# Kernel tuning notes

Hardware: AMD Instinct MI355X
Metric: run time of the kernel (lower is better)

## Reference

```python
import jax, jax.numpy as jnp
import numpy as np

N = 200000      # nodes per graph
E = 6400000     # edges per graph
F_IN = 100      # node feature dim (GCNConv(100,16))
HID = 16
NC = 2
STRIDE = 20     # log_softmax(...)[::20]
M = N // STRIDE # rows fed to the MLP head


def _gcn(x, src, dst, W1, b1, W2, b2):
    """PyG-style GCNConv x2: add self loops, sym-normalize, linear -> aggregate -> bias."""
    n = x.shape[0]
    loops = jnp.arange(n)
    s = jnp.concatenate([src, loops])
    d = jnp.concatenate([dst, loops])
    deg = jax.ops.segment_sum(jnp.ones(s.shape[0], dtype=x.dtype), d, num_segments=n)
    dinv = jnp.where(deg > 0, jax.lax.rsqrt(deg), 0.0)
    norm = (dinv[s] * dinv[d])[:, None]  # [E+n, 1]
    h = x @ W1                                    # [n, 16]
    h = jax.ops.segment_sum(norm * h[s], d, num_segments=n) + b1
    h = jax.nn.relu(h)  # dropout is identity in eval mode
    h = h @ W2                                    # [n, 2]
    h = jax.ops.segment_sum(norm * h[s], d, num_segments=n) + b2
    return jax.nn.log_softmax(h, axis=1)[::STRIDE]  # [n/20, 2]


def setup_inputs() -> dict:
    key = jax.random.key(0)
    ks = jax.random.split(key, 24)
    inp = {
        'batch1_edge_index': jax.random.randint(ks[0], (2, E), 0, N),
        'batch1_x': jax.random.normal(ks[1], (N, F_IN), dtype=jnp.float32),
        'batch2_edge_index': jax.random.randint(ks[2], (2, E), 0, N),
        'batch2_x': jax.random.normal(ks[3], (N, F_IN), dtype=jnp.float32),
        'transE_input': jax.random.uniform(ks[4], (M,), dtype=jnp.float32),
        'ComplEx_input': jax.random.uniform(ks[5], (M,), dtype=jnp.float32),
        'path_input': jax.random.uniform(ks[6], (M,), dtype=jnp.float32),
        'edit_input': jax.random.uniform(ks[7], (M,), dtype=jnp.float32),
    }
    s = 0.1
    inp['gh_W1'] = jax.random.normal(ks[8], (F_IN, HID), dtype=jnp.float32) * s
    inp['gh_b1'] = jnp.zeros((HID,), dtype=jnp.float32)
    inp['gh_W2'] = jax.random.normal(ks[9], (HID, NC), dtype=jnp.float32) * s
    inp['gh_b2'] = jnp.zeros((NC,), dtype=jnp.float32)
    inp['gt_W1'] = jax.random.normal(ks[10], (F_IN, HID), dtype=jnp.float32) * s
    inp['gt_b1'] = jnp.zeros((HID,), dtype=jnp.float32)
    inp['gt_W2'] = jax.random.normal(ks[11], (HID, NC), dtype=jnp.float32) * s
    inp['gt_b2'] = jnp.zeros((NC,), dtype=jnp.float32)
    inp['m_W1'] = jax.random.normal(ks[12], (5, 80), dtype=jnp.float32) * s
    inp['m_b1'] = jnp.zeros((80,), dtype=jnp.float32)
    inp['m_W2'] = jax.random.normal(ks[13], (80, 10), dtype=jnp.float32) * s
    inp['m_b2'] = jnp.zeros((10,), dtype=jnp.float32)
    inp['m_W3'] = jax.random.normal(ks[14], (10, 1), dtype=jnp.float32) * s
    inp['m_b3'] = jnp.zeros((1,), dtype=jnp.float32)
    return inp


def reference(batch1_edge_index, batch1_x, batch2_edge_index, batch2_x,
              transE_input, ComplEx_input, path_input, edit_input,
              gh_W1, gh_b1, gh_W2, gh_b2,
              gt_W1, gt_b1, gt_W2, gt_b2,
              m_W1, m_b1, m_W2, m_b2, m_W3, m_b3):
    gcnh_out = _gcn(batch1_x, batch1_edge_index[0], batch1_edge_index[1],
                    gh_W1, gh_b1, gh_W2, gh_b2)
    # gcnt_out is computed in the original forward but never used in the output
    gcnt_out = _gcn(batch2_x, batch2_edge_index[0], batch2_edge_index[1],
                    gt_W1, gt_b1, gt_W2, gt_b2)
    BP_input = jnp.concatenate(
        [transE_input[:, None], ComplEx_input[:, None], path_input[:, None], gcnh_out], axis=1)  # [M, 5]
    # NOTE: original computes mean/std normalization then OVERWRITES it with
    # min_max_normalize(BP_input); we faithfully apply only global min-max.
    mn, mx = jnp.min(BP_input), jnp.max(BP_input)
    BP_norm = (BP_input - mn) / (mx - mn)
    h = jax.nn.relu(BP_norm @ m_W1 + m_b1)
    h = jax.nn.relu(h @ m_W2 + m_b2)
    out = jax.nn.sigmoid(h @ m_W3 + m_b3)  # [M, 1]
    return out
```

## Files before the change

### kernel.cpp

```cpp
#include <hip/hip_runtime.h>
#include <math.h>

#define NN 200000
#define NE 6400000
#define FIN 100
#define MR 10000
#define BSH 14
#define NBK 13
#define NSB 1563
#define EPB 4096
#define CAP1E 544768
#define SBB 133
#define CAP2E 4864
#define SCAP 360448
#define STCAP 5120

static __device__ __forceinline__ unsigned enc_f(float f){
  unsigned u = __float_as_uint(f);
  return (u & 0x80000000u) ? ~u : (u | 0x80000000u);
}
static __device__ __forceinline__ float dec_f(unsigned u){
  return (u & 0x80000000u) ? __uint_as_float(u ^ 0x80000000u) : __uint_as_float(~u);
}
static __device__ __forceinline__ unsigned short f2bf(float f){
  unsigned u = __float_as_uint(f);
  return (unsigned short)((u + 0x7fffu + ((u >> 16) & 1u)) >> 16);
}
static __device__ __forceinline__ float bf2f(unsigned short h){
  return __uint_as_float(((unsigned)h) << 16);
}
static __device__ __forceinline__ float bflo(unsigned u){ return bf2f((unsigned short)u); }
static __device__ __forceinline__ float bfhi(unsigned u){ return bf2f((unsigned short)(u>>16)); }

__global__ void k_init(int* bcur1, int* bcur2, float* gacc, unsigned* mm, unsigned* scnt){
  int i = blockIdx.x*blockDim.x + threadIdx.x;
  if(i < NBK) bcur1[i] = i*CAP1E;
  if(i < NSB) bcur2[i] = i*CAP2E;
  if(i < 2*MR) gacc[i] = 0.f;
  if(i == 0){ mm[0] = 0xFFFFFFFFu; mm[1] = 0u; scnt[0] = 0u; }
}

__global__ __launch_bounds__(256) void k_stageA(const int* __restrict__ src,
                                                const int* __restrict__ dst,
                                                int* __restrict__ bcur1,
                                                unsigned* __restrict__ bucket1){
  __shared__ unsigned stage[EPB];
  __shared__ unsigned char binOf[EPB];
  __shared__ int cnt[4][NBK];
  __shared__ int tot[NBK], bst[NBK], woff[4][NBK], gbase[NBK];
  int t = threadIdx.x;
  int w = t >> 6;
  int ebase = blockIdx.x*EPB;
  int nEdge = min(EPB, NE - ebase);
  if(t < 4*NBK) ((int*)cnt)[t] = 0;
  __syncthreads();
  unsigned pk[16]; int bb[16], rr[16];
  const int4* s4 = (const int4*)(src + ebase);
  const int4* d4 = (const int4*)(dst + ebase);
  #pragma unroll
  for(int j=0;j<4;j++){
    int q = t + j*256, eo = q*4;
    if(eo < nEdge){
      int4 s = s4[q]; int4 d = d4[q];
      int ds[4] = {d.x,d.y,d.z,d.w}, ss[4] = {s.x,s.y,s.z,s.w};
      #pragma unroll
      for(int k=0;k<4;k++){
        int b = ds[k]>>BSH;
        pk[j*4+k] = ((unsigned)(ds[k] & 16383) << 18) | (unsigned)ss[k];
        bb[j*4+k] = b;
        rr[j*4+k] = atomicAdd(&cnt[w][b], 1);
      }
    } else {
      rr[j*4+0]=rr[j*4+1]=rr[j*4+2]=rr[j*4+3] = -1;
    }
  }
  __syncthreads();
  if(t < NBK){
    int s = 0;
    #pragma unroll
    for(int wv=0; wv<4; wv++){ woff[wv][t] = s; s += cnt[wv][t]; }
    tot[t] = s;
  }
  __syncthreads();
  if(t == 0){
    int run = 0;
    #pragma unroll
    for(int b=0;b<NBK;b++){ bst[b] = run; run += tot[b]; }
  }
  __syncthreads();
  if(t < NBK && tot[t]) gbase[t] = atomicAdd(&bcur1[t], tot[t]);
  #pragma unroll
  for(int j=0;j<16;j++){
    if(rr[j] >= 0){
      int b = bb[j];
      int p = bst[b] + woff[w][b] + rr[j];
      stage[p] = pk[j]; binOf[p] = (unsigned char)b;
    }
  }
  __syncthreads();
  for(int k=t; k<nEdge; k+=256){
    int b = binOf[k];
    bucket1[gbase[b] + (k - bst[b])] = stage[k];
  }
}

__global__ __launch_bounds__(256) void k_stageB(const unsigned* __restrict__ bucket1,
                                                const int* __restrict__ bcur1,
                                                int* __restrict__ bcur2,
                                                unsigned* __restrict__ bucket2,
                                                unsigned* __restrict__ sed,
                                                unsigned* __restrict__ scnt){
  __shared__ unsigned stage[EPB];
  __shared__ unsigned char binOf[EPB];
  __shared__ int cnt[128], bst[128], gbase[128];
  __shared__ unsigned sbuf[384];
  __shared__ int slds, sgbase;
  int t = threadIdx.x;
  int b = blockIdx.x / SBB;
  int chunk = blockIdx.x % SBB;
  int cntb = bcur1[b] - b*CAP1E;
  int el = chunk*EPB;
  int nEdge = min(EPB, cntb - el);
  if(nEdge <= 0) return;
  if(t < 128) cnt[t] = 0;
  if(t == 0) slds = 0;
  __syncthreads();
  int t20 = (20 - (4*b) % 20) % 20;
  unsigned pk2[16]; int ln[16], rr[16];
  const uint4* e4 = (const uint4*)(bucket1 + (size_t)b*CAP1E + el);
  #pragma unroll
  for(int j=0;j<4;j++){
    int q = t + j*256, eo = q*4;
    uint4 e = make_uint4(0,0,0,0);
    if(eo < nEdge) e = e4[q];
    unsigned ev[4] = {e.x, e.y, e.z, e.w};
    #pragma unroll
    for(int k=0;k<4;k++){
      int idx = j*4+k;
      if(eo + k < nEdge){
        unsigned p = ev[k];
        unsigned dl14 = p >> 18;
        int bin = (int)(dl14 >> 7);
        pk2[idx] = ((dl14 & 127u) << 18) | (p & 0x3FFFFu);
        ln[idx] = bin;
        rr[idx] = atomicAdd(&cnt[bin], 1);
        if((int)(dl14 % 20u) == t20){
          int sp = atomicAdd(&slds, 1);
          if(sp < 384){
            unsigned sidx = (unsigned)((b*16384 + (int)dl14) / 20);
            sbuf[sp] = (sidx << 18) | (p & 0x3FFFFu);
          }
        }
      } else rr[idx] = -1;
    }
  }
  __syncthreads();
  if(t == 0){
    int run = 0;
    for(int i=0;i<128;i++){ bst[i] = run; run += cnt[i]; }
    if(slds > 384) slds = 384;
    sgbase = (slds > 0) ? (int)atomicAdd(scnt, (unsigned)slds) : 0;
  }
  __syncthreads();
  if(t < 128 && cnt[t]){
    int sbg = (b<<7) + t;
    gbase[t] = atomicAdd(&bcur2[sbg], cnt[t]);
  }
  #pragma unroll
  for(int j=0;j<16;j++){
    if(rr[j] >= 0){
      int p = bst[ln[j]] + rr[j];
      stage[p] = pk2[j]; binOf[p] = (unsigned char)ln[j];
    }
  }
  __syncthreads();
  for(int k=t; k<nEdge; k+=256){
    int bin = binOf[k];
    bucket2[gbase[bin] + (k - bst[bin])] = stage[k];
  }
  for(int k=t; k<slds; k+=256){
    int gp = sgbase + k;
    if(gp < SCAP) sed[gp] = sbuf[k];
  }
}

__global__ __launch_bounds__(256) void k_cnt(const unsigned* __restrict__ bucket2,
                                             const int* __restrict__ bcur2,
                                             float* __restrict__ dinv){
  __shared__ int c[128];
  int sb = blockIdx.x, t = threadIdx.x;
  if(t < 128) c[t] = 0;
  __syncthreads();
  int e0 = sb*CAP2E, e1 = bcur2[sb];
  for(int i=e0+t; i<e1; i+=256){
    unsigned pkv = bucket2[i];
    atomicAdd(&c[pkv>>18], 1);
  }
  __syncthreads();
  if(t < 128){
    int g = sb*128 + t;
    if(g < NN) dinv[g] = rsqrtf((float)(c[t] + 1));
  }
}

__global__ __launch_bounds__(256) void k_xw1(const float* __restrict__ x,
                                             const float* __restrict__ W1,
                                             const float* __restrict__ dinv,
                                             unsigned short* __restrict__ h1b){
  int row = blockIdx.x*256 + threadIdx.x;
  if(row >= NN) return;
  const float4* xr = (const float4*)(x + (size_t)row*FIN);
  float acc[16];
  #pragma unroll
  for(int c=0;c<16;c++) acc[c] = 0.f;
  #pragma unroll 5
  for(int kk=0;kk<25;kk++){
    float4 xv = xr[kk];
    const float* w = W1 + kk*4*16;
    #pragma unroll
    for(int c=0;c<16;c++){
      acc[c] += xv.x*w[c] + xv.y*w[16+c] + xv.z*w[32+c] + xv.w*w[48+c];
    }
  }
  float dv = dinv[row];
  unsigned p[8];
  #pragma unroll
  for(int c=0;c<8;c++){
    p[c] = (unsigned)f2bf(acc[2*c]*dv) | ((unsigned)f2bf(acc[2*c+1]*dv) << 16);
  }
  uint4* o = (uint4*)(h1b + (size_t)row*16);
  o[0] = make_uint4(p[0],p[1],p[2],p[3]);
  o[1] = make_uint4(p[4],p[5],p[6],p[7]);
}

__global__ __launch_bounds__(512) void k_aggfused(const unsigned* __restrict__ bucket2,
                                                  const int* __restrict__ bcur2,
                                                  const float* __restrict__ dinv,
                                                  const unsigned short* __restrict__ h1b,
                                                  const float* __restrict__ b1,
                                                  const float* __restrict__ W2,
                                                  float* __restrict__ h2s){
  __shared__ unsigned srt[STCAP];
  __shared__ int cnt[128], coff[129], cur[128];
  __shared__ int wsum0;
  int t = threadIdx.x, sb = blockIdx.x;
  int e0 = sb*CAP2E, e1 = bcur2[sb];
  int n  = e1 - e0;
  bool ok = (n <= STCAP);
  if(t < 128) cnt[t] = 0;
  __syncthreads();

  if(ok){
    unsigned er[10];
    #pragma unroll
    for(int k=0;k<10;k++){
      int i = e0 + t + k*512;
      if(i < e1){
        unsigned p = bucket2[i];
        er[k] = p;
        atomicAdd(&cnt[p>>18], 1);
      } else er[k] = 0xFFFFFFFFu;
    }
    __syncthreads();
    int v = (t<128) ? cnt[t] : 0;
    int s = v;
    #pragma unroll
    for(int o=1;o<64;o<<=1){
      int u = __shfl_up(s, o, 64);
      if((t&63) >= o) s += u;
    }
    if(t == 63) wsum0 = s;
    __syncthreads();
    if(t < 128){
      int ex = s - v + ((t>=64) ? wsum0 : 0);
      coff[t] = ex; cur[t] = ex;
    }
    if(t == 0) coff[128] = n;
    __syncthreads();
    #pragma unroll
    for(int k=0;k<10;k++){
      if(er[k] != 0xFFFFFFFFu){
        int p = atomicAdd(&cur[er[k]>>18], 1);
        srt[p] = er[k] & 0x3FFFFu;
      }
    }
    __syncthreads();

    int node = t>>2, q = (t>>1)&1, f = t&1;
    int g = sb*128 + node;
    bool live = (g < NN);
    int s0 = 0, s1 = 0;
    if(live){ s0 = coff[node]; s1 = coff[node+1]; }
    int ne = s1 - s0;
    int mid = s0 + ((ne+1)>>1);
    int jb = q ? mid : s0;
    int je = q ? s1 : mid;
    const uint4* h1q = (const uint4*)h1b;
    float acc[8];
    #pragma unroll
    for(int c=0;c<8;c++) acc[c] = 0.f;
    if(live && q==0){
      uint4 su = h1q[(size_t)g*2 + f];
      acc[0]=bflo(su.x); acc[1]=bfhi(su.x); acc[2]=bflo(su.y); acc[3]=bfhi(su.y);
      acc[4]=bflo(su.z); acc[5]=bfhi(su.z); acc[6]=bflo(su.w); acc[7]=bfhi(su.w);
    }
    if(live){
      int j = jb;
      for(; j+4 <= je; j+=4){
        unsigned a0=srt[j], a1=srt[j+1], a2=srt[j+2], a3=srt[j+3];
        uint4 u0=h1q[a0*2+f], u1=h1q[a1*2+f], u2=h1q[a2*2+f], u3=h1q[a3*2+f];
        acc[0] += (bflo(u0.x)+bflo(u1.x)) + (bflo(u2.x)+bflo(u3.x));
        acc[1] += (bfhi(u0.x)+bfhi(u1.x)) + (bfhi(u2.x)+bfhi(u3.x));
        acc[2] += (bflo(u0.y)+bflo(u1.y)) + (bflo(u2.y)+bflo(u3.y));
        acc[3] += (bfhi(u0.y)+bfhi(u1.y)) + (bfhi(u2.y)+bfhi(u3.y));
        acc[4] += (bflo(u0.z)+bflo(u1.z)) + (bflo(u2.z)+bflo(u3.z));
        acc[5] += (bfhi(u0.z)+bfhi(u1.z)) + (bfhi(u2.z)+bfhi(u3.z));
        acc[6] += (bflo(u0.w)+bflo(u1.w)) + (bflo(u2.w)+bflo(u3.w));
        acc[7] += (bfhi(u0.w)+bfhi(u1.w)) + (bfhi(u2.w)+bfhi(u3.w));
      }
      for(; j<je; j++){
        uint4 u = h1q[srt[j]*2+f];
        acc[0]+=bflo(u.x); acc[1]+=bfhi(u.x); acc[2]+=bflo(u.y); acc[3]+=bfhi(u.y);
        acc[4]+=bflo(u.z); acc[5]+=bfhi(u.z); acc[6]+=bflo(u.w); acc[7]+=bfhi(u.w);
      }
    }
    #pragma unroll
    for(int c=0;c<8;c++) acc[c] += __shfl_xor(acc[c], 2, 4);
    if(live){
      float dvd = dinv[g];
      float p0 = 0.f, p1 = 0.f;
      #pragma unroll
      for(int c=0;c<8;c++){
        int fc = f*8 + c;
        float r = fmaxf(dvd*acc[c] + b1[fc], 0.f);
        p0 += r*W2[fc*2+0];
        p1 += r*W2[fc*2+1];
      }
      p0 += __shfl_xor(p0, 1, 4);
      p1 += __shfl_xor(p1, 1, 4);
      if((t&3) == 0){
        h2s[g*2+0] = dvd * p0;
        h2s[g*2+1] = dvd * p1;
      }
    }
  } else {
    float* accf = (float*)srt;
    for(int i=t; i<2048; i+=512) accf[i] = 0.f;
    __syncthreads();
    int grp = t>>4, f = t&15;
    for(int i=e0+grp; i<e1; i+=32){
      unsigned pkv = bucket2[i];
      atomicAdd(&accf[(pkv>>18)*16 + f], bf2f(h1b[(size_t)(pkv & 0x3FFFFu)*16 + f]));
    }
    __syncthreads();
    for(int nd=grp; nd<128; nd+=32){
      int g = sb*128 + nd;
      if(g >= NN) continue;
      float dvd = dinv[g];
      float acc = accf[nd*16 + f] + bf2f(h1b[(size_t)g*16 + f]);
      float r = fmaxf(dvd*acc + b1[f], 0.f);
      float p0 = r * W2[f*2+0];
      float p1 = r * W2[f*2+1];
      #pragma unroll
      for(int o=8;o>0;o>>=1){
        p0 += __shfl_xor(p0, o, 16);
        p1 += __shfl_xor(p1, o, 16);
      }
      if(f == 0){
        h2s[g*2+0] = dvd * p0;
        h2s[g*2+1] = dvd * p1;
      }
    }
  }
}

__global__ __launch_bounds__(256) void k_agg2s(const unsigned* __restrict__ sed,
                                               const unsigned* __restrict__ scnt,
                                               const float* __restrict__ h2s,
                                               float* __restrict__ gacc){
  int total = (int)scnt[0];
  if(total > SCAP) total = SCAP;
  const float2* h2v = (const float2*)h2s;
  for(int i = blockIdx.x*256 + threadIdx.x; i < total; i += gridDim.x*256){
    unsigned p = sed[i];
    int idx = (int)(p >> 18);
    int srcn = (int)(p & 0x3FFFFu);
    float2 v = h2v[srcn];
    atomicAdd(&gacc[idx*2+0], v.x);
    atomicAdd(&gacc[idx*2+1], v.y);
  }
}

__global__ __launch_bounds__(256) void k_post(const float* __restrict__ gacc,
                                              const float* __restrict__ h2s,
                                              const float* __restrict__ dinv,
                                              const float* __restrict__ b2,
                                              const float* __restrict__ t1,
                                              const float* __restrict__ t2,
                                              const float* __restrict__ t3,
                                              float* __restrict__ gout,
                                              unsigned* __restrict__ mm){
  int i = blockIdx.x*256 + threadIdx.x;
  float lo = 3.4e38f, hi = -3.4e38f;
  if(i < MR){
    int g = i*20;
    float dvd = dinv[g];
    float o0 = dvd*(gacc[i*2+0] + h2s[g*2+0]) + b2[0];
    float o1 = dvd*(gacc[i*2+1] + h2s[g*2+1]) + b2[1];
    float m = fmaxf(o0, o1);
    float lse = m + logf(expf(o0-m) + expf(o1-m));
    float g0 = o0 - lse, g1 = o1 - lse;
    gout[i*2+0] = g0; gout[i*2+1] = g1;
    float a = t1[i], bb = t2[i], c = t3[i];
    lo = fminf(fminf(a,bb), fminf(c, fminf(g0,g1)));
    hi = fmaxf(fmaxf(a,bb), fmaxf(c, fmaxf(g0,g1)));
  }
  #pragma unroll
  for(int o=32;o>0;o>>=1){
    lo = fminf(lo, __shfl_xor(lo, o, 64));
    hi = fmaxf(hi, __shfl_xor(hi, o, 64));
  }
  __shared__ float slo[4], shi[4];
  int w = threadIdx.x >> 6, l = threadIdx.x & 63;
  if(l == 0){ slo[w] = lo; shi[w] = hi; }
  __syncthreads();
  if(threadIdx.x == 0){
    for(int j=1;j<4;j++){ lo = fminf(lo, slo[j]); hi = fmaxf(hi, shi[j]); }
    atomicMin(&mm[0], enc_f(lo));
    atomicMax(&mm[1], enc_f(hi));
  }
}

__global__ __launch_bounds__(256) void k_mlp(const float* __restrict__ t1, const float* __restrict__ t2,
                                             const float* __restrict__ t3, const float* __restrict__ g,
                                             const unsigned* __restrict__ mm,
                                             const float* __restrict__ W1, const float* __restrict__ b1,
                                             const float* __restrict__ W2, const float* __restrict__ b2,
                                             const float* __restrict__ W3, const float* __restrict__ b3,
                                             float* __restrict__ out){
  int i = blockIdx.x*256 + threadIdx.x;
  if(i >= MR) return;
  float mn = dec_f(mm[0]), mx = dec_f(mm[1]);
  float sc = 1.f/(mx - mn);
  float in[5];
  in[0] = (t1[i]   - mn)*sc;
  in[1] = (t2[i]   - mn)*sc;
  in[2] = (t3[i]   - mn)*sc;
  in[3] = (g[2*i]  - mn)*sc;
  in[4] = (g[2*i+1]- mn)*sc;
  float a[80];
  #pragma unroll
  for(int j=0;j<80;j++){
    float s = b1[j];
    #pragma unroll
    for(int k=0;k<5;k++) s += in[k]*W1[k*80+j];
    a[j] = fmaxf(s, 0.f);
  }
  float h[10];
  #pragma unroll
  for(int j=0;j<10;j++){
    float s = b2[j];
    #pragma unroll
    for(int k=0;k<80;k++) s += a[k]*W2[k*10+j];
    h[j] = fmaxf(s, 0.f);
  }
  float o = b3[0];
  #pragma unroll
  for(int k=0;k<10;k++) o += h[k]*W3[k];
  out[i] = 1.f/(1.f + expf(-o));
}

extern "C" void kernel_launch(void* const* d_in, const int* in_sizes, int n_in,
                              void* d_out, int out_size, void* d_ws, size_t ws_size,
                              hipStream_t stream) {
  (void)in_sizes; (void)n_in; (void)out_size; (void)ws_size;
  const int*   eidx    = (const int*)  d_in[0];
  const int*   src     = eidx;
  const int*   dst     = eidx + NE;
  const float* x       = (const float*)d_in[1];
  const float* transE  = (const float*)d_in[4];
  const float* ComplEx = (const float*)d_in[5];
  const float* path    = (const float*)d_in[6];
  const float* ghW1    = (const float*)d_in[8];
  const float* ghb1    = (const float*)d_in[9];
  const float* ghW2    = (const float*)d_in[10];
  const float* ghb2    = (const float*)d_in[11];
  const float* mW1     = (const float*)d_in[16];
  const float* mb1     = (const float*)d_in[17];
  const float* mW2     = (const float*)d_in[18];
  const float* mb2     = (const float*)d_in[19];
  const float* mW3     = (const float*)d_in[20];
  const float* mb3     = (const float*)d_in[21];
  float* out = (float*)d_out;

  char* w = (char*)d_ws;
  size_t off = 0;
  auto alloc = [&](size_t bytes)->void*{
    void* p = w + off;
    off += (bytes + 255) & ~(size_t)255;
    return p;
  };
  unsigned* bucket1 = (unsigned*)alloc((size_t)NBK*CAP1E*4);
  unsigned* bucket2 = (unsigned*)alloc((size_t)NSB*CAP2E*4);
  float*    dinv    = (float*)   alloc((size_t)NN*4);
  unsigned short* h1b = (unsigned short*)alloc((size_t)NN*16*2);
  float*    h2s     = (float*)   alloc((size_t)NN*2*4);
  float*    gacc    = (float*)   alloc((size_t)MR*2*4);
  float*    gout    = (float*)   alloc((size_t)MR*2*4);
  unsigned* sed     = (unsigned*)alloc((size_t)SCAP*4);
  int*      bcur1   = (int*)     alloc(64*4);
  int*      bcur2   = (int*)     alloc((size_t)(NSB+1)*4);
  unsigned* mm      = (unsigned*)alloc(256);
  unsigned* scnt    = (unsigned*)alloc(256);

  const int SA_BLOCKS = (NE + EPB - 1)/EPB;
  const int SB_BLOCKS = NBK*SBB;

  k_init    <<<(2*MR+255)/256, 256, 0, stream>>>(bcur1, bcur2, gacc, mm, scnt);
  k_stageA  <<<SA_BLOCKS, 256, 0, stream>>>(src, dst, bcur1, bucket1);
  k_stageB  <<<SB_BLOCKS, 256, 0, stream>>>(bucket1, bcur1, bcur2, bucket2, sed, scnt);
  k_cnt     <<<NSB, 256, 0, stream>>>(bucket2, bcur2, dinv);
  k_xw1     <<<(NN+255)/256, 256, 0, stream>>>(x, ghW1, dinv, h1b);
  k_aggfused<<<NSB, 512, 0, stream>>>(bucket2, bcur2, dinv, h1b, ghb1, ghW2, h2s);
  k_agg2s   <<<512, 256, 0, stream>>>(sed, scnt, h2s, gacc);
  k_post    <<<(MR+255)/256, 256, 0, stream>>>(gacc, h2s, dinv, ghb2,
                                               transE, ComplEx, path, gout, mm);
  k_mlp     <<<(MR+255)/256, 256, 0, stream>>>(transE, ComplEx, path, gout, mm,
                                               mW1, mb1, mW2, mb2, mW3, mb3, out);
}
```

Baseline: 447.1 us.

## Compute degrees with global atomics in stageA and drop the separate count kernel

Measured after the change: 658.8 us. 47.4% more time.

```diff
diff --git a/kernel.cpp b/kernel.cpp
--- a/kernel.cpp
+++ b/kernel.cpp
@@ -32,18 +32,21 @@
 static __device__ __forceinline__ float bflo(unsigned u){ return bf2f((unsigned short)u); }
 static __device__ __forceinline__ float bfhi(unsigned u){ return bf2f((unsigned short)(u>>16)); }
 
-__global__ void k_init(int* bcur1, int* bcur2, float* gacc, unsigned* mm, unsigned* scnt){
+__global__ void k_init(int* bcur1, int* bcur2, float* gacc, unsigned* mm, unsigned* scnt,
+                       int* deg){
   int i = blockIdx.x*blockDim.x + threadIdx.x;
   if(i < NBK) bcur1[i] = i*CAP1E;
   if(i < NSB) bcur2[i] = i*CAP2E;
   if(i < 2*MR) gacc[i] = 0.f;
+  if(i < NN) deg[i] = 0;
   if(i == 0){ mm[0] = 0xFFFFFFFFu; mm[1] = 0u; scnt[0] = 0u; }
 }
 
 __global__ __launch_bounds__(256) void k_stageA(const int* __restrict__ src,
                                                 const int* __restrict__ dst,
                                                 int* __restrict__ bcur1,
-                                                unsigned* __restrict__ bucket1){
+                                                unsigned* __restrict__ bucket1,
+                                                int* __restrict__ deg){
   __shared__ unsigned stage[EPB];
   __shared__ unsigned char binOf[EPB];
   __shared__ int cnt[4][NBK];
@@ -69,6 +72,7 @@
         pk[j*4+k] = ((unsigned)(ds[k] & 16383) << 18) | (unsigned)ss[k];
         bb[j*4+k] = b;
         rr[j*4+k] = atomicAdd(&cnt[w][b], 1);
+        atomicAdd(&deg[ds[k]], 1);
       }
     } else {
       rr[j*4+0]=rr[j*4+1]=rr[j*4+2]=rr[j*4+3] = -1;
@@ -184,28 +188,9 @@
   }
 }
 
-__global__ __launch_bounds__(256) void k_cnt(const unsigned* __restrict__ bucket2,
-                                             const int* __restrict__ bcur2,
-                                             float* __restrict__ dinv){
-  __shared__ int c[128];
-  int sb = blockIdx.x, t = threadIdx.x;
-  if(t < 128) c[t] = 0;
-  __syncthreads();
-  int e0 = sb*CAP2E, e1 = bcur2[sb];
-  for(int i=e0+t; i<e1; i+=256){
-    unsigned pkv = bucket2[i];
-    atomicAdd(&c[pkv>>18], 1);
-  }
-  __syncthreads();
-  if(t < 128){
-    int g = sb*128 + t;
-    if(g < NN) dinv[g] = rsqrtf((float)(c[t] + 1));
-  }
-}
-
 __global__ __launch_bounds__(256) void k_xw1(const float* __restrict__ x,
                                              const float* __restrict__ W1,
-                                             const float* __restrict__ dinv,
+                                             const int* __restrict__ deg,
                                              unsigned short* __restrict__ h1b){
   int row = blockIdx.x*256 + threadIdx.x;
   if(row >= NN) return;
@@ -222,7 +207,7 @@
       acc[c] += xv.x*w[c] + xv.y*w[16+c] + xv.z*w[32+c] + xv.w*w[48+c];
     }
   }
-  float dv = dinv[row];
+  float dv = rsqrtf((float)(deg[row] + 1));
   unsigned p[8];
   #pragma unroll
   for(int c=0;c<8;c++){
@@ -235,7 +220,6 @@
 
 __global__ __launch_bounds__(512) void k_aggfused(const unsigned* __restrict__ bucket2,
                                                   const int* __restrict__ bcur2,
-                                                  const float* __restrict__ dinv,
                                                   const unsigned short* __restrict__ h1b,
                                                   const float* __restrict__ b1,
                                                   const float* __restrict__ W2,
@@ -327,7 +311,7 @@
     #pragma unroll
     for(int c=0;c<8;c++) acc[c] += __shfl_xor(acc[c], 2, 4);
     if(live){
-      float dvd = dinv[g];
+      float dvd = rsqrtf((float)(ne + 1));
       float p0 = 0.f, p1 = 0.f;
       #pragma unroll
       for(int c=0;c<8;c++){
@@ -344,6 +328,8 @@
       }
     }
   } else {
+    for(int i=e0+t; i<e1; i+=512) atomicAdd(&cnt[bucket2[i]>>18], 1);
+    __syncthreads();
     float* accf = (float*)srt;
     for(int i=t; i<2048; i+=512) accf[i] = 0.f;
     __syncthreads();
@@ -356,7 +342,7 @@
     for(int nd=grp; nd<128; nd+=32){
       int g = sb*128 + nd;
       if(g >= NN) continue;
-      float dvd = dinv[g];
+      float dvd = rsqrtf((float)(cnt[nd] + 1));
       float acc = accf[nd*16 + f] + bf2f(h1b[(size_t)g*16 + f]);
       float r = fmaxf(dvd*acc + b1[f], 0.f);
       float p0 = r * W2[f*2+0];
@@ -393,7 +379,7 @@
 
 __global__ __launch_bounds__(256) void k_post(const float* __restrict__ gacc,
                                               const float* __restrict__ h2s,
-                                              const float* __restrict__ dinv,
+                                              const int* __restrict__ deg,
                                               const float* __restrict__ b2,
                                               const float* __restrict__ t1,
                                               const float* __restrict__ t2,
@@ -404,7 +390,7 @@
   float lo = 3.4e38f, hi = -3.4e38f;
   if(i < MR){
     int g = i*20;
-    float dvd = dinv[g];
+    float dvd = rsqrtf((float)(deg[g] + 1));
     float o0 = dvd*(gacc[i*2+0] + h2s[g*2+0]) + b2[0];
     float o1 = dvd*(gacc[i*2+1] + h2s[g*2+1]) + b2[1];
     float m = fmaxf(o0, o1);
@@ -502,7 +488,7 @@
   };
   unsigned* bucket1 = (unsigned*)alloc((size_t)NBK*CAP1E*4);
   unsigned* bucket2 = (unsigned*)alloc((size_t)NSB*CAP2E*4);
-  float*    dinv    = (float*)   alloc((size_t)NN*4);
+  int*      deg     = (int*)     alloc((size_t)NN*4);
   unsigned short* h1b = (unsigned short*)alloc((size_t)NN*16*2);
   float*    h2s     = (float*)   alloc((size_t)NN*2*4);
   float*    gacc    = (float*)   alloc((size_t)MR*2*4);
@@ -516,14 +502,13 @@
   const int SA_BLOCKS = (NE + EPB - 1)/EPB;
   const int SB_BLOCKS = NBK*SBB;
 
-  k_init    <<<(2*MR+255)/256, 256, 0, stream>>>(bcur1, bcur2, gacc, mm, scnt);
-  k_stageA  <<<SA_BLOCKS, 256, 0, stream>>>(src, dst, bcur1, bucket1);
+  k_init    <<<(NN+255)/256, 256, 0, stream>>>(bcur1, bcur2, gacc, mm, scnt, deg);
+  k_stageA  <<<SA_BLOCKS, 256, 0, stream>>>(src, dst, bcur1, bucket1, deg);
   k_stageB  <<<SB_BLOCKS, 256, 0, stream>>>(bucket1, bcur1, bcur2, bucket2, sed, scnt);
-  k_cnt     <<<NSB, 256, 0, stream>>>(bucket2, bcur2, dinv);
-  k_xw1     <<<(NN+255)/256, 256, 0, stream>>>(x, ghW1, dinv, h1b);
-  k_aggfused<<<NSB, 512, 0, stream>>>(bucket2, bcur2, dinv, h1b, ghb1, ghW2, h2s);
+  k_xw1     <<<(NN+255)/256, 256, 0, stream>>>(x, ghW1, deg, h1b);
+  k_aggfused<<<NSB, 512, 0, stream>>>(bucket2, bcur2, h1b, ghb1, ghW2, h2s);
   k_agg2s   <<<512, 256, 0, stream>>>(sed, scnt, h2s, gacc);
-  k_post    <<<(MR+255)/256, 256, 0, stream>>>(gacc, h2s, dinv, ghb2,
+  k_post    <<<(MR+255)/256, 256, 0, stream>>>(gacc, h2s, deg, ghb2,
                                                transE, ComplEx, path, gout, mm);
   k_mlp     <<<(MR+255)/256, 256, 0, stream>>>(transE, ComplEx, path, gout, mm,
                                                mW1, mb1, mW2, mb2, mW3, mb3, out);
```
